# Performance work log

Hardware: AMD Instinct MI355X
Metric: run time of the kernel (lower is better)

Reference implementation:

```python
import jax, jax.numpy as jnp
import numpy as np

EPS = 1e-6

def setup_inputs() -> dict:
    key = jax.random.key(0)
    ks = jax.random.split(key, 5)
    B, H, N, D = 4, 8, 8192, 64
    q = jax.random.uniform(ks[0], (B, H, N, D), dtype=jnp.float32)
    k = jax.random.uniform(ks[1], (B, H, N, D), dtype=jnp.float32)
    q_rot = jax.random.uniform(ks[2], (B, H, N, D), dtype=jnp.float32)
    k_rot = jax.random.uniform(ks[3], (B, H, N, D), dtype=jnp.float32)
    v = jax.random.normal(ks[4], (B, H, N, D), dtype=jnp.float32)
    return {"q": q, "k": k, "q_rot": q_rot, "k_rot": k_rot, "v": v, "chunk_size": 128}


def _chunked_causal_linear_attention(q, k, q_rot, k_rot, v, chunk_size):
    # Faithful port of infer_hidden_states: chunked causal linear attention
    # with cumsum kernel trick and recurrent state carry-over.
    B, H, N, D = q.shape
    E = v.shape[-1]
    C = chunk_size
    nc = N // C

    def to_chunks(x):
        # [B,H,N,d] -> [nc,B,H,C,d]
        return jnp.moveaxis(x.reshape(B, H, nc, C, x.shape[-1]), 2, 0)

    qc, kc, qrc, krc, vc = map(to_chunks, (q, k, q_rot, k_rot, v))

    init = (
        jnp.zeros((B, H, 1, D), q.dtype),        # last_k_cumsum
        jnp.zeros((B, H, 1, D, E), q.dtype),     # last_context_cumsum
        jnp.zeros((B, H, 1, D), q.dtype),        # last_k_cumsum_rot
        jnp.zeros((B, H, 1, D, E), q.dtype),     # last_context_cumsum_rot
    )

    def step(carry, inp):
        last_k, last_S, last_k_rot, last_S_rot = carry
        qi, ki, qri, kri, vi = inp                  # [B,H,C,*]
        k_cs = last_k + jnp.cumsum(ki, axis=-2)     # [B,H,C,D]
        k_cs_rot = last_k_rot + jnp.cumsum(kri, axis=-2)
        Dn = jnp.einsum('bhnd,bhnd->bhn', qi, k_cs)
        Dr = jnp.einsum('bhnd,bhnd->bhn', qri, k_cs_rot)
        D_inv = 1.0 / (Dn + Dr + EPS)               # [B,H,C]
        ctx = jnp.einsum('bhnd,bhne->bhnde', ki, vi)
        S = last_S + jnp.cumsum(ctx, axis=2)        # [B,H,C,D,E]
        ctx_rot = jnp.einsum('bhnd,bhne->bhnde', kri, vi)
        S_rot = last_S_rot + jnp.cumsum(ctx_rot, axis=2)
        out = jnp.einsum('bhnde,bhnd,bhn->bhne', S, qi, D_inv)
        out = out + jnp.einsum('bhnde,bhnd,bhn->bhne', S_rot, qri, D_inv)
        new_carry = (k_cs[:, :, -1:], S[:, :, -1:], k_cs_rot[:, :, -1:], S_rot[:, :, -1:])
        return new_carry, out

    (Z, S, Z_rot, S_rot), outs = jax.lax.scan(step, init, (qc, kc, qrc, krc, vc))
    out = jnp.moveaxis(outs, 0, 2).reshape(B, H, N, E)
    # states: squeeze chunk dim as in torch (squeeze(2))
    return out, Z[:, :, 0], S[:, :, 0], Z_rot[:, :, 0], S_rot[:, :, 0]


def reference(q, k, q_rot, k_rot, v, chunk_size):
    return _chunked_causal_linear_attention(q, k, q_rot, k_rot, v, chunk_size)
```

## Files before the change

### kernel.cpp

```cpp
#include <hip/hip_runtime.h>


typedef short bf16x8 __attribute__((ext_vector_type(8)));
typedef float f32x4  __attribute__((ext_vector_type(4)));

constexpr int B_ = 4, H_ = 8, BH = 32;
constexpr int N_ = 8192, D_ = 64, E_ = 64, C_ = 128;
constexpr int NC = 64;
constexpr int NCHUNKS = BH * NC;
constexpr int STATE = 64 + 64 + 64 * 64 + 64 * 64;
#define EPS_ 1e-6f

constexpr size_t OUT_ELEMS = (size_t)BH * N_ * E_;
constexpr size_t ZOFF  = OUT_ELEMS;
constexpr size_t SOFF  = ZOFF  + (size_t)BH * 64;
constexpr size_t ZROFF = SOFF  + (size_t)BH * 4096;
constexpr size_t SROFF = ZROFF + (size_t)BH * 64;

__device__ inline unsigned cvt2(float a, float b){
    union { float f; unsigned u; } x, y; x.f = a; y.f = b;
    unsigned lo = (x.u + 0x7fffu + ((x.u >> 16) & 1u)) >> 16;
    unsigned hi = (y.u + 0x7fffu + ((y.u >> 16) & 1u)) >> 16;
    return lo | (hi << 16);
}
__device__ inline unsigned short cvt1(float a){
    union { float f; unsigned u; } x; x.f = a;
    return (unsigned short)((x.u + 0x7fffu + ((x.u >> 16) & 1u)) >> 16);
}

__global__ __launch_bounds__(256) void chunk_states(
    const float* __restrict__ gk, const float* __restrict__ gkr,
    const float* __restrict__ gv, float* __restrict__ ws)
{
    __shared__ float sk[32][68], skr[32][68], sv[32][68];
    const int t = threadIdx.x;
    const int cid = blockIdx.x;
    const int bh = cid >> 6;
    const int c  = cid & 63;
    const size_t gbase = (size_t)bh * N_ * D_ + (size_t)c * C_ * D_;

    const int d2 = t >> 3;
    const int e0 = (t & 7) * 8;

    float acc0[8], acc1[8], accr0[8], accr1[8];
#pragma unroll
    for (int j = 0; j < 8; ++j) { acc0[j]=0.f; acc1[j]=0.f; accr0[j]=0.f; accr1[j]=0.f; }
    float sumk = 0.f;

    for (int mt = 0; mt < 4; ++mt) {
        const int m0 = mt * 32;
#pragma unroll
        for (int i = 0; i < 2; ++i) {
            int fi = i * 256 + t;
            int row = fi >> 4, c4 = (fi & 15) * 4;
            const size_t g = gbase + (size_t)(m0 + row) * D_ + c4;
            *(float4*)&sk [row][c4] = *(const float4*)(gk  + g);
            *(float4*)&skr[row][c4] = *(const float4*)(gkr + g);
            *(float4*)&sv [row][c4] = *(const float4*)(gv  + g);
        }
        __syncthreads();
#pragma unroll 4
        for (int m = 0; m < 32; ++m) {
            const float kd0  = sk [m][d2], kd1  = sk [m][d2 + 32];
            const float krd0 = skr[m][d2], krd1 = skr[m][d2 + 32];
            const float4 va = *(const float4*)&sv[m][e0];
            const float4 vb = *(const float4*)&sv[m][e0 + 4];
            const float vv[8] = {va.x,va.y,va.z,va.w, vb.x,vb.y,vb.z,vb.w};
#pragma unroll
            for (int j = 0; j < 8; ++j) {
                acc0 [j] += kd0  * vv[j];
                acc1 [j] += kd1  * vv[j];
                accr0[j] += krd0 * vv[j];
                accr1[j] += krd1 * vv[j];
            }
        }
        if (t < 64) {
            for (int m = 0; m < 32; ++m) sumk += sk[m][t];
        } else if (t < 128) {
            const int d = t - 64;
            for (int m = 0; m < 32; ++m) sumk += skr[m][d];
        }
        __syncthreads();
    }

    float* st = ws + (size_t)cid * STATE;
    if (t < 128) st[t] = sumk;
    float* cs  = st + 128;
    float* csr = st + 128 + 64 * 64;
    *(float4*)&cs [d2 * 64 + e0]            = make_float4(acc0[0], acc0[1], acc0[2], acc0[3]);
    *(float4*)&cs [d2 * 64 + e0 + 4]        = make_float4(acc0[4], acc0[5], acc0[6], acc0[7]);
    *(float4*)&cs [(d2 + 32) * 64 + e0]     = make_float4(acc1[0], acc1[1], acc1[2], acc1[3]);
    *(float4*)&cs [(d2 + 32) * 64 + e0 + 4] = make_float4(acc1[4], acc1[5], acc1[6], acc1[7]);
    *(float4*)&csr[d2 * 64 + e0]            = make_float4(accr0[0], accr0[1], accr0[2], accr0[3]);
    *(float4*)&csr[d2 * 64 + e0 + 4]        = make_float4(accr0[4], accr0[5], accr0[6], accr0[7]);
    *(float4*)&csr[(d2 + 32) * 64 + e0]     = make_float4(accr1[0], accr1[1], accr1[2], accr1[3]);
    *(float4*)&csr[(d2 + 32) * 64 + e0 + 4] = make_float4(accr1[4], accr1[5], accr1[6], accr1[7]);
}

__global__ __launch_bounds__(256) void scan_states(float* __restrict__ ws, float* __restrict__ out)
{
    const int bh = blockIdx.x;
    const int j  = blockIdx.y * 256 + threadIdx.x;
    if (j >= STATE) return;
    float run = 0.f;
    const size_t base = (size_t)bh * NC * STATE + j;
#pragma unroll 4
    for (int c = 0; c < NC; ++c) {
        const size_t idx = base + (size_t)c * STATE;
        const float x = ws[idx];
        ws[idx] = run;
        run += x;
    }
    if (j < 64)        out[ZOFF  + (size_t)bh * 64   + j]          = run;
    else if (j < 128)  out[ZROFF + (size_t)bh * 64   + (j - 64)]   = run;
    else if (j < 4224) out[SOFF  + (size_t)bh * 4096 + (j - 128)]  = run;
    else               out[SROFF + (size_t)bh * 4096 + (j - 4224)] = run;
}

constexpr int TILE = 520;
constexpr int SQ0  = 0;
constexpr int SK0  = 8320;
constexpr int SV0  = 16640;
constexpr int SSC0 = 8320;
constexpr int SP0  = 20800;
constexpr int SM_TOT = 24960;

#define MFMA(A,B,C) __builtin_amdgcn_mfma_f32_16x16x32_bf16((A),(B),(C),0,0,0)

__device__ inline void stage_row(const float* p, unsigned short* dst, int r, int c0, int mr, int mc){
    float4 f0 = ((const float4*)p)[0], f1 = ((const float4*)p)[1];
    float4 f2 = ((const float4*)p)[2], f3 = ((const float4*)p)[3];
    int tile = (r >> 4) * mr + (c0 >> 5) * mc;
    int g0   = (c0 & 31) >> 3;
    uint4 u0 = make_uint4(cvt2(f0.x,f0.y), cvt2(f0.z,f0.w), cvt2(f1.x,f1.y), cvt2(f1.z,f1.w));
    uint4 u1 = make_uint4(cvt2(f2.x,f2.y), cvt2(f2.z,f2.w), cvt2(f3.x,f3.y), cvt2(f3.z,f3.w));
    *(uint4*)&dst[tile*TILE + ((r&15) + 16* g0   )*8] = u0;
    *(uint4*)&dst[tile*TILE + ((r&15) + 16*(g0+1))*8] = u1;
}

__device__ inline void stage_colT(const float* src, int ldr, unsigned short* dst, int mr, int mc){
    const int t = threadIdx.x;
    const int col = t & 63, r0 = (t >> 6) * 16;
    float v[16];
#pragma unroll
    for (int i = 0; i < 16; ++i) v[i] = src[(size_t)(r0 + i) * ldr + col];
#pragma unroll
    for (int h = 0; h < 2; ++h) {
        int rr = r0 + 8 * h;
        int tile = (rr >> 5) * mr + (col >> 4) * mc;
        uint4 u = make_uint4(cvt2(v[8*h+0],v[8*h+1]), cvt2(v[8*h+2],v[8*h+3]),
                             cvt2(v[8*h+4],v[8*h+5]), cvt2(v[8*h+6],v[8*h+7]));
        *(uint4*)&dst[tile*TILE + ((col&15) + 16*((rr&31)>>3))*8] = u;
    }
}

__global__ __launch_bounds__(256, 3) void chunk_out(
    const float* __restrict__ gq, const float* __restrict__ gqr,
    const float* __restrict__ gk, const float* __restrict__ gkr,
    const float* __restrict__ gv, const float* __restrict__ ws,
    float* __restrict__ out)
{
    __shared__ unsigned short sm[SM_TOT];
    const int t = threadIdx.x;
    const int blk = blockIdx.x, chunk = blk >> 1, rb = blk & 1;
    const int bh = chunk >> 6, c = chunk & 63;
    const size_t gbase = (size_t)bh * N_ * D_ + (size_t)c * C_ * D_;
    const float* st = ws + (size_t)chunk * STATE;
    const int w = t >> 6, lane = t & 63, lg = lane >> 4, lm = lane & 15;

    {
        const int r = t >> 2, c0 = (t & 3) * 16;
        const size_t g = gbase + (size_t)rb * 64 * D_ + (size_t)r * D_ + c0;
        stage_row(gq  + g, sm + SQ0,            r, c0, 2, 1);
        stage_row(gqr + g, sm + SQ0 + 8 * TILE, r, c0, 2, 1);
    }

    f32x4 oacc[4];
#pragma unroll
    for (int te = 0; te < 4; ++te) oacc[te] = f32x4{0.f, 0.f, 0.f, 0.f};
    f32x4 acc4 = f32x4{0.f, 0.f, 0.f, 0.f};
    float denp[4] = {0.f, 0.f, 0.f, 0.f};
    bf16x8 qf[2][2];

    const int TMmax = rb * 4 + w;
    const int TKtop = ((TMmax >> 1) << 1) + 1;

#define KFRG(ten,td,tm)  (*(const bf16x8*)&sm[SK0  + (((ten)*2+(td))*4+(tm))*TILE + lane*8])
#define VFRG(tk,te)      (*(const bf16x8*)&sm[SV0  + ((tk)*4+(te))*TILE + lane*8])
#define SCFRG(ten,td,te) (*(const bf16x8*)&sm[SSC0 + ((ten)*10+(td)*5+(te))*TILE + lane*8])

    for (int mh = 0; mh < 2; ++mh) {
        __syncthreads();
        if (mh == 0 || rb == 1) {
            const int r = t >> 2, c0 = (t & 3) * 16;
            const size_t kg = gbase + (size_t)mh * 64 * D_ + (size_t)r * D_ + c0;
            stage_row(gk  + kg, sm + SK0,            r, c0, 1, 4);
            stage_row(gkr + kg, sm + SK0 + 8 * TILE, r, c0, 1, 4);
            stage_colT(gv + gbase + (size_t)mh * 64 * D_, D_, sm + SV0, 4, 1);
        }
        __syncthreads();
        if (mh == 0) {
#pragma unroll
            for (int td = 0; td < 2; ++td) {
                qf[0][td] = *(const bf16x8*)&sm[SQ0 +            (w*2+td)*TILE + lane*8];
                qf[1][td] = *(const bf16x8*)&sm[SQ0 + 8*TILE +   (w*2+td)*TILE + lane*8];
            }
        }
        if (mh == 0 || rb == 1) {
#pragma unroll
            for (int tm = 0; tm < 4; ++tm) {
                const int TM = mh * 4 + tm;
                if (TM <= TKtop) {
                    f32x4 a = f32x4{0.f, 0.f, 0.f, 0.f};
                    if (TM <= TMmax) {
                        a = MFMA(qf[0][0], KFRG(0,0,tm), a);
                        a = MFMA(qf[0][1], KFRG(0,1,tm), a);
                        a = MFMA(qf[1][0], KFRG(1,0,tm), a);
                        a = MFMA(qf[1][1], KFRG(1,1,tm), a);
                    }
                    const int mb = TM * 16 + lm;
                    const int pb = SP0 + (w*2 + (tm>>1))*TILE
                                 + 16*((tm&1)*2 + (lm>>3))*8 + (lm&7);
#pragma unroll
                    for (int r = 0; r < 4; ++r) {
                        const int ng = rb*64 + w*16 + lg*4 + r;
                        const float pv = (TM <= TMmax && mb <= ng) ? a[r] : 0.f;
                        denp[r] += pv;
                        sm[pb + (lg*4 + r)*8] = cvt1(pv);
                    }
                }
            }
#pragma unroll
            for (int tk = 0; tk < 2; ++tk) {
                const int TK = mh * 2 + tk;
                if (TK <= (TMmax >> 1)) {
                    bf16x8 pa = *(const bf16x8*)&sm[SP0 + (w*2+tk)*TILE + lane*8];
#pragma unroll
                    for (int te = 0; te < 4; ++te)
                        oacc[te] = MFMA(pa, VFRG(tk,te), oacc[te]);
                }
            }
        }
    }

    __syncthreads();
    stage_colT(st + 128,        64, sm + SSC0,             5, 1);
    stage_colT(st + 128 + 4096, 64, sm + SSC0 + 10 * TILE, 5, 1);
    for (int i = t; i < 4 * 260; i += 256) {
        int tile = i / 260, off = i % 260;
        int ten = tile >> 1, td = tile & 1;
        *(unsigned*)&sm[SSC0 + (ten*10 + td*5 + 4)*TILE + off*2] = 0u;
    }
    __syncthreads();
    if (t < 128) {
        int ten = t >> 6, d = t & 63;
        sm[SSC0 + (ten*10 + (d>>5)*5 + 4)*TILE + (16*((d&31)>>3))*8 + (d&7)] = cvt1(st[t]);
    }
    __syncthreads();
#pragma unroll
    for (int td = 0; td < 2; ++td) {
#pragma unroll
        for (int te = 0; te < 4; ++te) {
            oacc[te] = MFMA(qf[0][td], SCFRG(0,td,te), oacc[te]);
            oacc[te] = MFMA(qf[1][td], SCFRG(1,td,te), oacc[te]);
        }
        acc4 = MFMA(qf[0][td], SCFRG(0,td,4), acc4);
        acc4 = MFMA(qf[1][td], SCFRG(1,td,4), acc4);
    }

    const size_t orow = (size_t)bh * N_ * E_ + (size_t)(c * C_ + rb * 64 + w * 16) * E_;
#pragma unroll
    for (int r = 0; r < 4; ++r) {
        float d = denp[r];
        d += __shfl_xor(d, 1); d += __shfl_xor(d, 2);
        d += __shfl_xor(d, 4); d += __shfl_xor(d, 8);
        const float dc = __shfl(acc4[r], lane & 48);
        const float dinv = 1.0f / (d + dc + EPS_);
        const size_t ob = orow + (size_t)(lg * 4 + r) * E_ + lm;
        out[ob +  0] = oacc[0][r] * dinv;
        out[ob + 16] = oacc[1][r] * dinv;
        out[ob + 32] = oacc[2][r] * dinv;
        out[ob + 48] = oacc[3][r] * dinv;
    }
#undef KFRG
#undef VFRG
#undef SCFRG
}

extern "C" void kernel_launch(void* const* d_in, const int* in_sizes, int n_in,
                              void* d_out, int out_size, void* d_ws, size_t ws_size,
                              hipStream_t stream) {
    const float* q  = (const float*)d_in[0];
    const float* k  = (const float*)d_in[1];
    const float* qr = (const float*)d_in[2];
    const float* kr = (const float*)d_in[3];
    const float* v  = (const float*)d_in[4];
    float* out = (float*)d_out;
    float* ws  = (float*)d_ws;

    chunk_states<<<NCHUNKS, 256, 0, stream>>>(k, kr, v, ws);
    scan_states<<<dim3(BH, 33), 256, 0, stream>>>(ws, out);
    chunk_out<<<NCHUNKS * 2, 256, 0, stream>>>(q, qr, k, kr, v, ws, out);
}
```

Baseline: 401.0 us.

## Move chunk-state accumulation to split-bf16 MFMA and restructure output kernel staging

The chunk_states kernel now computes the per-chunk k^T v and key sums with bf16 MFMA, splitting each fp32 input into high and low bf16 parts (three products) to keep near-fp32 accuracy, where it previously used scalar FMA. The key sums come from an MFMA against a ones matrix. scan_states is vectorised to float4 with fewer blocks. chunk_out loads q fragments straight from global into registers, drops the q staging area to shrink shared memory, raises occupancy to 4 blocks, and prefetches the second K half into registers. Several ideas are combined, and the split-bf16 path adds conversion work and some accuracy risk.

```diff
diff --git a/kernel.cpp b/kernel.cpp
--- a/kernel.cpp
+++ b/kernel.cpp
@@ -3,12 +3,13 @@
 
 typedef short bf16x8 __attribute__((ext_vector_type(8)));
 typedef float f32x4  __attribute__((ext_vector_type(4)));
-
-constexpr int B_ = 4, H_ = 8, BH = 32;
+union U16x8 { bf16x8 v; uint4 u; };
+
+constexpr int BH = 32;
 constexpr int N_ = 8192, D_ = 64, E_ = 64, C_ = 128;
 constexpr int NC = 64;
 constexpr int NCHUNKS = BH * NC;
-constexpr int STATE = 64 + 64 + 64 * 64 + 64 * 64;
+constexpr int STATE = 8320;
 #define EPS_ 1e-6f
 
 constexpr size_t OUT_ELEMS = (size_t)BH * N_ * E_;
@@ -27,116 +28,152 @@
     union { float f; unsigned u; } x; x.f = a;
     return (unsigned short)((x.u + 0x7fffu + ((x.u >> 16) & 1u)) >> 16);
 }
-
-__global__ __launch_bounds__(256) void chunk_states(
+__device__ inline float bflo(float x, unsigned short hi){
+    union { unsigned u; float f; } h; h.u = ((unsigned)hi) << 16;
+    return x - h.f;
+}
+
+constexpr int TILE = 520;
+#define MFMA(A,B,C) __builtin_amdgcn_mfma_f32_16x16x32_bf16((A),(B),(C),0,0,0)
+
+constexpr int AKH = 0, AKL = 8, ARH = 16, ARL = 24, BVH = 32, BVL = 40, BON = 48;
+constexpr int SM1_TOT = 50 * TILE;
+
+__global__ __launch_bounds__(256, 3) void chunk_states(
     const float* __restrict__ gk, const float* __restrict__ gkr,
     const float* __restrict__ gv, float* __restrict__ ws)
 {
-    __shared__ float sk[32][68], skr[32][68], sv[32][68];
+    __shared__ unsigned short sm[SM1_TOT];
     const int t = threadIdx.x;
-    const int cid = blockIdx.x;
-    const int bh = cid >> 6;
-    const int c  = cid & 63;
+    const int cid = blockIdx.x, bh = cid >> 6, c = cid & 63;
     const size_t gbase = (size_t)bh * N_ * D_ + (size_t)c * C_ * D_;
-
-    const int d2 = t >> 3;
-    const int e0 = (t & 7) * 8;
-
-    float acc0[8], acc1[8], accr0[8], accr1[8];
-#pragma unroll
-    for (int j = 0; j < 8; ++j) { acc0[j]=0.f; acc1[j]=0.f; accr0[j]=0.f; accr1[j]=0.f; }
-    float sumk = 0.f;
-
-    for (int mt = 0; mt < 4; ++mt) {
-        const int m0 = mt * 32;
-#pragma unroll
-        for (int i = 0; i < 2; ++i) {
-            int fi = i * 256 + t;
-            int row = fi >> 4, c4 = (fi & 15) * 4;
-            const size_t g = gbase + (size_t)(m0 + row) * D_ + c4;
-            *(float4*)&sk [row][c4] = *(const float4*)(gk  + g);
-            *(float4*)&skr[row][c4] = *(const float4*)(gkr + g);
-            *(float4*)&sv [row][c4] = *(const float4*)(gv  + g);
-        }
-        __syncthreads();
-#pragma unroll 4
-        for (int m = 0; m < 32; ++m) {
-            const float kd0  = sk [m][d2], kd1  = sk [m][d2 + 32];
-            const float krd0 = skr[m][d2], krd1 = skr[m][d2 + 32];
-            const float4 va = *(const float4*)&sv[m][e0];
-            const float4 vb = *(const float4*)&sv[m][e0 + 4];
-            const float vv[8] = {va.x,va.y,va.z,va.w, vb.x,vb.y,vb.z,vb.w};
+    const int w = t >> 6, lane = t & 63, lg = lane >> 4, lm = lane & 15;
+    const int col = t & 63, r0g = (t >> 6) * 16;
+
+    float kv[16], krv[16], vv[16];
+    auto load_half = [&](int h){
+        const size_t base = gbase + (size_t)(h * 64 + r0g) * D_ + col;
+#pragma unroll
+        for (int i = 0; i < 16; ++i) {
+            kv [i] = gk [base + (size_t)i * D_];
+            krv[i] = gkr[base + (size_t)i * D_];
+            vv [i] = gv [base + (size_t)i * D_];
+        }
+    };
+    auto write_hl = [&](const float* v16, int hiT, int loT){
+#pragma unroll
+        for (int hh = 0; hh < 2; ++hh) {
+            const int rr = r0g + 8 * hh;
+            const int tile = (rr >> 5) * 4 + (col >> 4);
+            const int off = ((col & 15) + 16 * ((rr & 31) >> 3)) * 8;
+            unsigned short h8[8]; float l8[8];
 #pragma unroll
             for (int j = 0; j < 8; ++j) {
-                acc0 [j] += kd0  * vv[j];
-                acc1 [j] += kd1  * vv[j];
-                accr0[j] += krd0 * vv[j];
-                accr1[j] += krd1 * vv[j];
+                h8[j] = cvt1(v16[8*hh + j]);
+                l8[j] = bflo(v16[8*hh + j], h8[j]);
             }
-        }
-        if (t < 64) {
-            for (int m = 0; m < 32; ++m) sumk += sk[m][t];
-        } else if (t < 128) {
-            const int d = t - 64;
-            for (int m = 0; m < 32; ++m) sumk += skr[m][d];
-        }
-        __syncthreads();
-    }
+            uint4 uh = make_uint4((unsigned)h8[0] | ((unsigned)h8[1] << 16),
+                                  (unsigned)h8[2] | ((unsigned)h8[3] << 16),
+                                  (unsigned)h8[4] | ((unsigned)h8[5] << 16),
+                                  (unsigned)h8[6] | ((unsigned)h8[7] << 16));
+            uint4 ul = make_uint4(cvt2(l8[0],l8[1]), cvt2(l8[2],l8[3]),
+                                  cvt2(l8[4],l8[5]), cvt2(l8[6],l8[7]));
+            *(uint4*)&sm[(hiT + tile) * TILE + off] = uh;
+            *(uint4*)&sm[(loT + tile) * TILE + off] = ul;
+        }
+    };
+
+    for (int i = t; i < 2 * TILE; i += 256) {
+        const int tile = i / TILE, off = i % TILE;
+        unsigned short val = (off < 512 && ((off >> 3) & 15) == 0) ? (unsigned short)0x3F80 : (unsigned short)0;
+        sm[(BON + tile) * TILE + off] = val;
+    }
+
+    f32x4 aK[4], aR[4], sK = {0.f,0.f,0.f,0.f}, sR = {0.f,0.f,0.f,0.f};
+#pragma unroll
+    for (int e = 0; e < 4; ++e) { aK[e] = f32x4{0.f,0.f,0.f,0.f}; aR[e] = f32x4{0.f,0.f,0.f,0.f}; }
+
+    auto FR = [&](int tile)->bf16x8 { return *(const bf16x8*)&sm[tile * TILE + lane * 8]; };
+    auto compute = [&](){
+#pragma unroll
+        for (int kt = 0; kt < 2; ++kt) {
+            bf16x8 ah = FR(AKH + kt*4 + w), al = FR(AKL + kt*4 + w);
+            bf16x8 rh = FR(ARH + kt*4 + w), rl = FR(ARL + kt*4 + w);
+            bf16x8 bo = FR(BON + kt);
+            sK = MFMA(ah, bo, sK); sK = MFMA(al, bo, sK);
+            sR = MFMA(rh, bo, sR); sR = MFMA(rl, bo, sR);
+#pragma unroll
+            for (int et = 0; et < 4; ++et) {
+                bf16x8 bh = FR(BVH + kt*4 + et), bl = FR(BVL + kt*4 + et);
+                aK[et] = MFMA(ah, bh, aK[et]);
+                aK[et] = MFMA(al, bh, aK[et]);
+                aK[et] = MFMA(ah, bl, aK[et]);
+                aR[et] = MFMA(rh, bh, aR[et]);
+                aR[et] = MFMA(rl, bh, aR[et]);
+                aR[et] = MFMA(rh, bl, aR[et]);
+            }
+        }
+    };
+
+    load_half(0);
+    write_hl(kv, AKH, AKL); write_hl(krv, ARH, ARL); write_hl(vv, BVH, BVL);
+    load_half(1);
+    __syncthreads();
+    compute();
+    __syncthreads();
+    write_hl(kv, AKH, AKL); write_hl(krv, ARH, ARL); write_hl(vv, BVH, BVL);
+    __syncthreads();
+    compute();
 
     float* st = ws + (size_t)cid * STATE;
-    if (t < 128) st[t] = sumk;
+    if (lm == 0) {
+#pragma unroll
+        for (int r = 0; r < 4; ++r) {
+            const int d = w*16 + lg*4 + r;
+            st[d]      = sK[r];
+            st[64 + d] = sR[r];
+        }
+    }
     float* cs  = st + 128;
-    float* csr = st + 128 + 64 * 64;
-    *(float4*)&cs [d2 * 64 + e0]            = make_float4(acc0[0], acc0[1], acc0[2], acc0[3]);
-    *(float4*)&cs [d2 * 64 + e0 + 4]        = make_float4(acc0[4], acc0[5], acc0[6], acc0[7]);
-    *(float4*)&cs [(d2 + 32) * 64 + e0]     = make_float4(acc1[0], acc1[1], acc1[2], acc1[3]);
-    *(float4*)&cs [(d2 + 32) * 64 + e0 + 4] = make_float4(acc1[4], acc1[5], acc1[6], acc1[7]);
-    *(float4*)&csr[d2 * 64 + e0]            = make_float4(accr0[0], accr0[1], accr0[2], accr0[3]);
-    *(float4*)&csr[d2 * 64 + e0 + 4]        = make_float4(accr0[4], accr0[5], accr0[6], accr0[7]);
-    *(float4*)&csr[(d2 + 32) * 64 + e0]     = make_float4(accr1[0], accr1[1], accr1[2], accr1[3]);
-    *(float4*)&csr[(d2 + 32) * 64 + e0 + 4] = make_float4(accr1[4], accr1[5], accr1[6], accr1[7]);
+    float* csr = st + 128 + 4096;
+#pragma unroll
+    for (int et = 0; et < 4; ++et)
+#pragma unroll
+        for (int r = 0; r < 4; ++r) {
+            const int d = w*16 + lg*4 + r, e = et*16 + lm;
+            cs [d*64 + e] = aK[et][r];
+            csr[d*64 + e] = aR[et][r];
+        }
 }
 
 __global__ __launch_bounds__(256) void scan_states(float* __restrict__ ws, float* __restrict__ out)
 {
     const int bh = blockIdx.x;
-    const int j  = blockIdx.y * 256 + threadIdx.x;
-    if (j >= STATE) return;
-    float run = 0.f;
-    const size_t base = (size_t)bh * NC * STATE + j;
-#pragma unroll 4
+    const int j4 = blockIdx.y * 256 + threadIdx.x;
+    if (j4 >= STATE / 4) return;
+    float4 run = make_float4(0.f, 0.f, 0.f, 0.f);
+    float* base = ws + (size_t)bh * NC * STATE + (size_t)j4 * 4;
+#pragma unroll 8
     for (int c = 0; c < NC; ++c) {
-        const size_t idx = base + (size_t)c * STATE;
-        const float x = ws[idx];
-        ws[idx] = run;
-        run += x;
-    }
-    if (j < 64)        out[ZOFF  + (size_t)bh * 64   + j]          = run;
-    else if (j < 128)  out[ZROFF + (size_t)bh * 64   + (j - 64)]   = run;
-    else if (j < 4224) out[SOFF  + (size_t)bh * 4096 + (j - 128)]  = run;
-    else               out[SROFF + (size_t)bh * 4096 + (j - 4224)] = run;
-}
-
-constexpr int TILE = 520;
-constexpr int SQ0  = 0;
-constexpr int SK0  = 8320;
-constexpr int SV0  = 16640;
-constexpr int SSC0 = 8320;
-constexpr int SP0  = 20800;
-constexpr int SM_TOT = 24960;
-
-#define MFMA(A,B,C) __builtin_amdgcn_mfma_f32_16x16x32_bf16((A),(B),(C),0,0,0)
-
-__device__ inline void stage_row(const float* p, unsigned short* dst, int r, int c0, int mr, int mc){
-    float4 f0 = ((const float4*)p)[0], f1 = ((const float4*)p)[1];
-    float4 f2 = ((const float4*)p)[2], f3 = ((const float4*)p)[3];
-    int tile = (r >> 4) * mr + (c0 >> 5) * mc;
-    int g0   = (c0 & 31) >> 3;
-    uint4 u0 = make_uint4(cvt2(f0.x,f0.y), cvt2(f0.z,f0.w), cvt2(f1.x,f1.y), cvt2(f1.z,f1.w));
-    uint4 u1 = make_uint4(cvt2(f2.x,f2.y), cvt2(f2.z,f2.w), cvt2(f3.x,f3.y), cvt2(f3.z,f3.w));
-    *(uint4*)&dst[tile*TILE + ((r&15) + 16* g0   )*8] = u0;
-    *(uint4*)&dst[tile*TILE + ((r&15) + 16*(g0+1))*8] = u1;
-}
+        float4 x = *(float4*)(base + (size_t)c * STATE);
+        *(float4*)(base + (size_t)c * STATE) = run;
+        run.x += x.x; run.y += x.y; run.z += x.z; run.w += x.w;
+    }
+    const int j = j4 * 4;
+    float* dst;
+    if (j < 64)        dst = out + ZOFF  + (size_t)bh*64   + j;
+    else if (j < 128)  dst = out + ZROFF + (size_t)bh*64   + (j - 64);
+    else if (j < 4224) dst = out + SOFF  + (size_t)bh*4096 + (j - 128);
+    else               dst = out + SROFF + (size_t)bh*4096 + (j - 4224);
+    *(float4*)dst = run;
+}
+
+constexpr int SK0 = 0, SV0 = 16, SP0 = 24, SSC0 = 0;
+constexpr int SM3_TOT = 32 * TILE;
+
+#define KFRG(ten,td,tm)  (*(const bf16x8*)&sm[(SK0 + ((ten)*2+(td))*4+(tm))*TILE + lane*8])
+#define VFRG(tk,te)      (*(const bf16x8*)&sm[(SV0 + (tk)*4+(te))*TILE + lane*8])
+#define SCFRG(ten,td,te) (*(const bf16x8*)&sm[(SSC0 + (ten)*10+(td)*5+(te))*TILE + lane*8])
 
 __device__ inline void stage_colT(const float* src, int ldr, unsigned short* dst, int mr, int mc){
     const int t = threadIdx.x;
@@ -146,115 +183,153 @@
     for (int i = 0; i < 16; ++i) v[i] = src[(size_t)(r0 + i) * ldr + col];
 #pragma unroll
     for (int h = 0; h < 2; ++h) {
-        int rr = r0 + 8 * h;
-        int tile = (rr >> 5) * mr + (col >> 4) * mc;
+        const int rr = r0 + 8 * h;
+        const int tile = (rr >> 5) * mr + (col >> 4) * mc;
         uint4 u = make_uint4(cvt2(v[8*h+0],v[8*h+1]), cvt2(v[8*h+2],v[8*h+3]),
                              cvt2(v[8*h+4],v[8*h+5]), cvt2(v[8*h+6],v[8*h+7]));
         *(uint4*)&dst[tile*TILE + ((col&15) + 16*((rr&31)>>3))*8] = u;
     }
 }
 
-__global__ __launch_bounds__(256, 3) void chunk_out(
+__global__ __launch_bounds__(256, 4) void chunk_out(
     const float* __restrict__ gq, const float* __restrict__ gqr,
     const float* __restrict__ gk, const float* __restrict__ gkr,
     const float* __restrict__ gv, const float* __restrict__ ws,
     float* __restrict__ out)
 {
-    __shared__ unsigned short sm[SM_TOT];
+    __shared__ unsigned short sm[SM3_TOT];
     const int t = threadIdx.x;
-    const int blk = blockIdx.x, chunk = blk >> 1, rb = blk & 1;
+    const int blk = blockIdx.x, chunk = blk >> 1, rbk = blk & 1;
     const int bh = chunk >> 6, c = chunk & 63;
     const size_t gbase = (size_t)bh * N_ * D_ + (size_t)c * C_ * D_;
     const float* st = ws + (size_t)chunk * STATE;
     const int w = t >> 6, lane = t & 63, lg = lane >> 4, lm = lane & 15;
-
+    const int col = t & 63, r0g = (t >> 6) * 16;
+
+    bf16x8 qf[2][2];
     {
+        const size_t qrow = gbase + (size_t)(rbk*64 + w*16 + lm) * D_;
+#pragma unroll
+        for (int td = 0; td < 2; ++td) {
+            const size_t g = qrow + td*32 + lg*8;
+            float4 a = *(const float4*)(gq + g),  b = *(const float4*)(gq + g + 4);
+            float4 ar= *(const float4*)(gqr + g), br= *(const float4*)(gqr + g + 4);
+            U16x8 u;
+            u.u = make_uint4(cvt2(a.x,a.y), cvt2(a.z,a.w), cvt2(b.x,b.y), cvt2(b.z,b.w));
+            qf[0][td] = u.v;
+            u.u = make_uint4(cvt2(ar.x,ar.y), cvt2(ar.z,ar.w), cvt2(br.x,br.y), cvt2(br.z,br.w));
+            qf[1][td] = u.v;
+        }
+    }
+
+    float4 kf4[4], rf4[4];
+    auto load_kr = [&](int mh){
+        const size_t g = gbase + (size_t)(mh*64 + (t >> 2)) * D_ + (t & 3)*16;
+#pragma unroll
+        for (int i = 0; i < 4; ++i) {
+            kf4[i] = *(const float4*)(gk  + g + i*4);
+            rf4[i] = *(const float4*)(gkr + g + i*4);
+        }
+    };
+    auto write_row_reg = [&](const float4* f, int baseT, int mr, int mc){
         const int r = t >> 2, c0 = (t & 3) * 16;
-        const size_t g = gbase + (size_t)rb * 64 * D_ + (size_t)r * D_ + c0;
-        stage_row(gq  + g, sm + SQ0,            r, c0, 2, 1);
-        stage_row(gqr + g, sm + SQ0 + 8 * TILE, r, c0, 2, 1);
-    }
+        const int tile = (r >> 4) * mr + (c0 >> 5) * mc;
+        const int g0 = (c0 & 31) >> 3;
+        uint4 u0 = make_uint4(cvt2(f[0].x,f[0].y), cvt2(f[0].z,f[0].w),
+                              cvt2(f[1].x,f[1].y), cvt2(f[1].z,f[1].w));
+        uint4 u1 = make_uint4(cvt2(f[2].x,f[2].y), cvt2(f[2].z,f[2].w),
+                              cvt2(f[3].x,f[3].y), cvt2(f[3].z,f[3].w));
+        *(uint4*)&sm[(baseT + tile)*TILE + ((r&15) + 16* g0   )*8] = u0;
+        *(uint4*)&sm[(baseT + tile)*TILE + ((r&15) + 16*(g0+1))*8] = u1;
+    };
+    auto stage_v = [&](int mh){
+        float vv[16];
+        const size_t base = gbase + (size_t)(mh*64 + r0g) * D_ + col;
+#pragma unroll
+        for (int i = 0; i < 16; ++i) vv[i] = gv[base + (size_t)i * D_];
+#pragma unroll
+        for (int hh = 0; hh < 2; ++hh) {
+            const int rr = r0g + 8*hh;
+            const int tile = (rr >> 5) * 4 + (col >> 4);
+            uint4 u = make_uint4(cvt2(vv[8*hh+0],vv[8*hh+1]), cvt2(vv[8*hh+2],vv[8*hh+3]),
+                                 cvt2(vv[8*hh+4],vv[8*hh+5]), cvt2(vv[8*hh+6],vv[8*hh+7]));
+            *(uint4*)&sm[(SV0 + tile)*TILE + ((col&15) + 16*((rr&31)>>3))*8] = u;
+        }
+    };
 
     f32x4 oacc[4];
 #pragma unroll
-    for (int te = 0; te < 4; ++te) oacc[te] = f32x4{0.f, 0.f, 0.f, 0.f};
-    f32x4 acc4 = f32x4{0.f, 0.f, 0.f, 0.f};
-    float denp[4] = {0.f, 0.f, 0.f, 0.f};
-    bf16x8 qf[2][2];
-
-    const int TMmax = rb * 4 + w;
+    for (int te = 0; te < 4; ++te) oacc[te] = f32x4{0.f,0.f,0.f,0.f};
+    f32x4 acc4 = f32x4{0.f,0.f,0.f,0.f};
+    float denp[4] = {0.f,0.f,0.f,0.f};
+
+    const int TMmax = rbk * 4 + w;
     const int TKtop = ((TMmax >> 1) << 1) + 1;
 
-#define KFRG(ten,td,tm)  (*(const bf16x8*)&sm[SK0  + (((ten)*2+(td))*4+(tm))*TILE + lane*8])
-#define VFRG(tk,te)      (*(const bf16x8*)&sm[SV0  + ((tk)*4+(te))*TILE + lane*8])
-#define SCFRG(ten,td,te) (*(const bf16x8*)&sm[SSC0 + ((ten)*10+(td)*5+(te))*TILE + lane*8])
-
-    for (int mh = 0; mh < 2; ++mh) {
-        __syncthreads();
-        if (mh == 0 || rb == 1) {
-            const int r = t >> 2, c0 = (t & 3) * 16;
-            const size_t kg = gbase + (size_t)mh * 64 * D_ + (size_t)r * D_ + c0;
-            stage_row(gk  + kg, sm + SK0,            r, c0, 1, 4);
-            stage_row(gkr + kg, sm + SK0 + 8 * TILE, r, c0, 1, 4);
-            stage_colT(gv + gbase + (size_t)mh * 64 * D_, D_, sm + SV0, 4, 1);
-        }
-        __syncthreads();
-        if (mh == 0) {
-#pragma unroll
-            for (int td = 0; td < 2; ++td) {
-                qf[0][td] = *(const bf16x8*)&sm[SQ0 +            (w*2+td)*TILE + lane*8];
-                qf[1][td] = *(const bf16x8*)&sm[SQ0 + 8*TILE +   (w*2+td)*TILE + lane*8];
-            }
-        }
-        if (mh == 0 || rb == 1) {
-#pragma unroll
-            for (int tm = 0; tm < 4; ++tm) {
-                const int TM = mh * 4 + tm;
-                if (TM <= TKtop) {
-                    f32x4 a = f32x4{0.f, 0.f, 0.f, 0.f};
-                    if (TM <= TMmax) {
-                        a = MFMA(qf[0][0], KFRG(0,0,tm), a);
-                        a = MFMA(qf[0][1], KFRG(0,1,tm), a);
-                        a = MFMA(qf[1][0], KFRG(1,0,tm), a);
-                        a = MFMA(qf[1][1], KFRG(1,1,tm), a);
-                    }
-                    const int mb = TM * 16 + lm;
-                    const int pb = SP0 + (w*2 + (tm>>1))*TILE
-                                 + 16*((tm&1)*2 + (lm>>3))*8 + (lm&7);
-#pragma unroll
-                    for (int r = 0; r < 4; ++r) {
-                        const int ng = rb*64 + w*16 + lg*4 + r;
-                        const float pv = (TM <= TMmax && mb <= ng) ? a[r] : 0.f;
-                        denp[r] += pv;
-                        sm[pb + (lg*4 + r)*8] = cvt1(pv);
-                    }
+    auto compute_half = [&](int mh){
+#pragma unroll
+        for (int tm = 0; tm < 4; ++tm) {
+            const int TM = mh*4 + tm;
+            if (TM <= TKtop) {
+                f32x4 a = f32x4{0.f,0.f,0.f,0.f};
+                if (TM <= TMmax) {
+                    a = MFMA(qf[0][0], KFRG(0,0,tm), a);
+                    a = MFMA(qf[0][1], KFRG(0,1,tm), a);
+                    a = MFMA(qf[1][0], KFRG(1,0,tm), a);
+                    a = MFMA(qf[1][1], KFRG(1,1,tm), a);
+                }
+                const int mb = TM * 16 + lm;
+                const int pb = (SP0 + w*2 + (tm>>1))*TILE
+                             + 16*((tm&1)*2 + (lm>>3))*8 + (lm&7);
+#pragma unroll
+                for (int r = 0; r < 4; ++r) {
+                    const int ng = rbk*64 + w*16 + lg*4 + r;
+                    const float pv = (TM <= TMmax && mb <= ng) ? a[r] : 0.f;
+                    denp[r] += pv;
+                    sm[pb + (lg*4 + r)*8] = cvt1(pv);
                 }
             }
-#pragma unroll
-            for (int tk = 0; tk < 2; ++tk) {
-                const int TK = mh * 2 + tk;
-                if (TK <= (TMmax >> 1)) {
-                    bf16x8 pa = *(const bf16x8*)&sm[SP0 + (w*2+tk)*TILE + lane*8];
-#pragma unroll
-                    for (int te = 0; te < 4; ++te)
-                        oacc[te] = MFMA(pa, VFRG(tk,te), oacc[te]);
-                }
+        }
+#pragma unroll
+        for (int tk = 0; tk < 2; ++tk) {
+            const int TK = mh*2 + tk;
+            if (TK <= (TMmax >> 1)) {
+                bf16x8 pa = *(const bf16x8*)&sm[(SP0 + w*2+tk)*TILE + lane*8];
+#pragma unroll
+                for (int te = 0; te < 4; ++te)
+                    oacc[te] = MFMA(pa, VFRG(tk,te), oacc[te]);
             }
         }
-    }
-
-    __syncthreads();
-    stage_colT(st + 128,        64, sm + SSC0,             5, 1);
-    stage_colT(st + 128 + 4096, 64, sm + SSC0 + 10 * TILE, 5, 1);
+    };
+
+    load_kr(0);
+    write_row_reg(kf4, SK0, 1, 4);
+    write_row_reg(rf4, SK0 + 8, 1, 4);
+    stage_v(0);
+    if (rbk) load_kr(1);
+    __syncthreads();
+    compute_half(0);
+    if (rbk) {
+        __syncthreads();
+        write_row_reg(kf4, SK0, 1, 4);
+        write_row_reg(rf4, SK0 + 8, 1, 4);
+        stage_v(1);
+        __syncthreads();
+        compute_half(1);
+    }
+
+    __syncthreads();
+    stage_colT(st + 128,        64, sm + SSC0*TILE,             5, 1);
+    stage_colT(st + 128 + 4096, 64, sm + (SSC0 + 10)*TILE,      5, 1);
     for (int i = t; i < 4 * 260; i += 256) {
-        int tile = i / 260, off = i % 260;
-        int ten = tile >> 1, td = tile & 1;
-        *(unsigned*)&sm[SSC0 + (ten*10 + td*5 + 4)*TILE + off*2] = 0u;
+        const int tile = i / 260, off = i % 260;
+        const int ten = tile >> 1, td = tile & 1;
+        *(unsigned*)&sm[(SSC0 + ten*10 + td*5 + 4)*TILE + off*2] = 0u;
     }
     __syncthreads();
     if (t < 128) {
-        int ten = t >> 6, d = t & 63;
-        sm[SSC0 + (ten*10 + (d>>5)*5 + 4)*TILE + (16*((d&31)>>3))*8 + (d&7)] = cvt1(st[t]);
+        const int ten = t >> 6, d = t & 63;
+        sm[(SSC0 + ten*10 + (d>>5)*5 + 4)*TILE + (16*((d&31)>>3))*8 + (d&7)] = cvt1(st[t]);
     }
     __syncthreads();
 #pragma unroll
@@ -268,7 +343,7 @@
         acc4 = MFMA(qf[1][td], SCFRG(1,td,4), acc4);
     }
 
-    const size_t orow = (size_t)bh * N_ * E_ + (size_t)(c * C_ + rb * 64 + w * 16) * E_;
+    const size_t orow = (size_t)bh * N_ * E_ + (size_t)(c * C_ + rbk * 64 + w * 16) * E_;
 #pragma unroll
     for (int r = 0; r < 4; ++r) {
         float d = denp[r];
@@ -282,10 +357,10 @@
         out[ob + 32] = oacc[2][r] * dinv;
         out[ob + 48] = oacc[3][r] * dinv;
     }
+}
 #undef KFRG
 #undef VFRG
 #undef SCFRG
-}
 
 extern "C" void kernel_launch(void* const* d_in, const int* in_sizes, int n_in,
                               void* d_out, int out_size, void* d_ws, size_t ws_size,
@@ -299,6 +374,6 @@
     float* ws  = (float*)d_ws;
 
     chunk_states<<<NCHUNKS, 256, 0, stream>>>(k, kr, v, ws);
-    scan_states<<<dim3(BH, 33), 256, 0, stream>>>(ws, out);
+    scan_states<<<dim3(BH, 9), 256, 0, stream>>>(ws, out);
     chunk_out<<<NCHUNKS * 2, 256, 0, stream>>>(q, qr, k, kr, v, ws, out);
 }
```

Result: no change. 398.4 us (-0.7%).
